# Kernel optimization log

Measured on AMD Instinct MI355X. Metric: run time of the kernel, lower is better.

The kernel has to match this reference:

```python
import jax, jax.numpy as jnp
import numpy as np

T = 2048        # q_len (current chunk)
P = 2048        # past KV cache length
HID = 4096      # hidden_size
H = 32          # num_attention_heads
D = HID // H    # head_dim = 128
THETA = 10000.0


def apply_rope(x, pos):
    # x: [H, T, D], pos: [T] int
    half = D // 2
    inv_freq = 1.0 / (THETA ** (jnp.arange(0, half, dtype=jnp.float32) / half))
    ang = pos.astype(jnp.float32)[:, None] * inv_freq[None, :]      # [T, D/2]
    cos = jnp.concatenate([jnp.cos(ang), jnp.cos(ang)], axis=-1)[None]  # [1, T, D]
    sin = jnp.concatenate([jnp.sin(ang), jnp.sin(ang)], axis=-1)[None]
    rot = jnp.concatenate([-x[..., half:], x[..., :half]], axis=-1)
    return x * cos + rot * sin


def setup_inputs() -> dict:
    key = jax.random.key(0)
    ks = jax.random.split(key, 8)
    s = 1.0 / np.sqrt(HID)
    inp = {
        "hidden_states": jax.random.normal(ks[0], (T, HID), dtype=jnp.float32),
        "attention_mask": jnp.triu(jnp.full((T, T), -jnp.inf, dtype=jnp.float32), k=1),
        "Wq": jax.random.normal(ks[1], (HID, HID), dtype=jnp.float32) * s,
        "Wk": jax.random.normal(ks[2], (HID, HID), dtype=jnp.float32) * s,
        "Wv": jax.random.normal(ks[3], (HID, HID), dtype=jnp.float32) * s,
        "Wo": jax.random.normal(ks[4], (HID, HID), dtype=jnp.float32) * s,
        "past_k": jax.random.normal(ks[5], (H, P, D), dtype=jnp.float32),
        "past_v": jax.random.normal(ks[6], (H, P, D), dtype=jnp.float32),
        "position_ids": P + jnp.arange(T, dtype=jnp.int32),
        "past_length": P,
    }
    return inp


def reference(hidden_states, attention_mask, Wq, Wk, Wv, Wo, past_k, past_v,
              position_ids, past_length):
    # QKV projections -> [H, T, D]
    proj = lambda W: (hidden_states @ W).reshape(T, H, D).transpose(1, 0, 2)
    q, k, v = proj(Wq), proj(Wk), proj(Wv)
    q = apply_rope(q, position_ids)
    k = apply_rope(k, position_ids)

    scale = 1.0 / jnp.sqrt(jnp.float32(D))
    # scores against past cache and current chunk (fp32 softmax, as in source)
    past_dots = (jnp.einsum('htd,hsd->hts', q, past_k) * scale).astype(jnp.float32)
    pmask = jnp.where(jnp.arange(P) < past_length, 0.0, -jnp.inf)  # [P]
    past_dots = past_dots + pmask
    cur = ((jnp.einsum('htd,hsd->hts', q, k) * scale) + attention_mask).astype(jnp.float32)

    # online-softmax merge via logsumexp combination
    past_lse = jax.scipy.special.logsumexp(past_dots, axis=-1, keepdims=True)
    cur_lse = jax.scipy.special.logsumexp(cur, axis=-1, keepdims=True)
    tot_lse = jnp.logaddexp(past_lse, cur_lse)
    pw = jnp.exp(past_dots - tot_lse).astype(q.dtype)
    cw = jnp.exp(cur - tot_lse).astype(q.dtype)

    out = jnp.einsum('hts,hsd->htd', pw, past_v) + jnp.einsum('hts,hsd->htd', cw, v)
    out = jnp.where(past_length == 0,
                    jnp.einsum('hts,hsd->htd', jax.nn.softmax(cur, axis=-1).astype(q.dtype), v),
                    out)
    out = out.transpose(1, 0, 2).reshape(T, HID)   # [T, hidden]
    return out @ Wo
```

## Files before the change

### kernel.cpp

```cpp
#include <hip/hip_runtime.h>
#include <cstdint>
#include <cstddef>

#define T_LEN 2048
#define PAST_MAX 2048
#define HID 4096
#define NHEAD 32
#define DHEAD 128

typedef __bf16 bf16_t;
typedef __bf16 bf16x4 __attribute__((ext_vector_type(4)));
typedef __bf16 bf16x8 __attribute__((ext_vector_type(8)));
typedef float  f32x4  __attribute__((ext_vector_type(4)));
typedef float  f32x16 __attribute__((ext_vector_type(16)));
typedef unsigned int u32x4 __attribute__((ext_vector_type(4)));

__device__ __forceinline__ void gload16(const void* g, void* l){
  __builtin_amdgcn_global_load_lds((const __attribute__((address_space(1))) void*)g,
                                   (__attribute__((address_space(3))) void*)l,
                                   16, 0, 0);
}

__device__ __forceinline__ unsigned pack_bf16(float a, float b){
  const unsigned ua = __builtin_bit_cast(unsigned short, (bf16_t)a);
  const unsigned ub = __builtin_bit_cast(unsigned short, (bf16_t)b);
  return ua | (ub << 16);
}

__global__ void cvt2_k(const float* __restrict__ a, bf16_t* __restrict__ ao,
                       const float* __restrict__ b, bf16_t* __restrict__ bo, int n4){
  int i = blockIdx.x * 256 + threadIdx.x;
  if (i < n4){
    const float4 v = ((const float4*)a)[i];
    bf16x4 o = { (bf16_t)v.x, (bf16_t)v.y, (bf16_t)v.z, (bf16_t)v.w };
    ((bf16x4*)ao)[i] = o;
  } else {
    i -= n4;
    const float4 v = ((const float4*)b)[i];
    bf16x4 o = { (bf16_t)v.x, (bf16_t)v.y, (bf16_t)v.z, (bf16_t)v.w };
    ((bf16x4*)bo)[i] = o;
  }
}

__global__ __launch_bounds__(256) void transpose2_k(const float* __restrict__ in,
                                                    bf16_t* __restrict__ out, int R, int C){
  __shared__ float tile[64][65];
  const int r0 = blockIdx.x << 6, c0 = blockIdx.y << 6;
  const size_t bo = (size_t)blockIdx.z * (size_t)R * (size_t)C;
  const int tx = threadIdx.x & 15, ty = threadIdx.x >> 4;
#pragma unroll
  for (int k = 0; k < 4; ++k){
    const float4 v = *(const float4*)(in + bo + (size_t)(r0 + ty + 16*k) * C + c0 + tx*4);
    float* tp = &tile[ty + 16*k][tx*4];
    tp[0] = v.x; tp[1] = v.y; tp[2] = v.z; tp[3] = v.w;
  }
  __syncthreads();
  const int rr0 = (threadIdx.x & 7) * 8;
  const int ccb = threadIdx.x >> 3;
#pragma unroll
  for (int k = 0; k < 2; ++k){
    const int cc = ccb + 32*k;
    bf16x8 o;
#pragma unroll
    for (int j = 0; j < 8; ++j) o[j] = (bf16_t)tile[rr0 + j][cc];
    *(bf16x8*)(out + bo + (size_t)(c0 + cc) * R + r0 + rr0) = o;
  }
}

__global__ __launch_bounds__(256) void transpose3_k(
    const float* __restrict__ s0, const float* __restrict__ s1, const float* __restrict__ s2,
    bf16_t* __restrict__ d0, bf16_t* __restrict__ d1, bf16_t* __restrict__ d2){
  __shared__ float tile[64][65];
  const float* in = (blockIdx.z == 0) ? s0 : (blockIdx.z == 1) ? s1 : s2;
  bf16_t* out = (blockIdx.z == 0) ? d0 : (blockIdx.z == 1) ? d1 : d2;
  const int r0 = blockIdx.x << 6, c0 = blockIdx.y << 6;
  const int tx = threadIdx.x & 15, ty = threadIdx.x >> 4;
#pragma unroll
  for (int k = 0; k < 4; ++k){
    const float4 v = *(const float4*)(in + (size_t)(r0 + ty + 16*k) * HID + c0 + tx*4);
    float* tp = &tile[ty + 16*k][tx*4];
    tp[0] = v.x; tp[1] = v.y; tp[2] = v.z; tp[3] = v.w;
  }
  __syncthreads();
  const int rr0 = (threadIdx.x & 7) * 8;
  const int ccb = threadIdx.x >> 3;
#pragma unroll
  for (int k = 0; k < 2; ++k){
    const int cc = ccb + 32*k;
    bf16x8 o;
#pragma unroll
    for (int j = 0; j < 8; ++j) o[j] = (bf16_t)tile[rr0 + j][cc];
    *(bf16x8*)(out + (size_t)(c0 + cc) * HID + r0 + rr0) = o;
  }
}

__global__ void ropek_k(bf16_t* __restrict__ K, const int* __restrict__ pos){
  const int idx = blockIdx.x * 256 + threadIdx.x;
  const int i = idx & 63;
  const int t = (idx >> 6) & (T_LEN - 1);
  const int h = idx >> 17;
  const size_t base = ((size_t)h * T_LEN + t) * DHEAD;
  const float p = (float)pos[t];
  const float inv = __expf(-(float)i * 0.14391156605212898f);
  const float ang = p * inv;
  float sn, cs;
  sincosf(ang, &sn, &cs);
  const float b0 = (float)K[base + i], b1 = (float)K[base + i + 64];
  K[base + i]      = (bf16_t)(b0 * cs - b1 * sn);
  K[base + i + 64] = (bf16_t)(b1 * cs + b0 * sn);
}

__global__ __launch_bounds__(512, 1) void gemmqkv256_k(
    const bf16_t* __restrict__ A,
    const bf16_t* __restrict__ B0, const bf16_t* __restrict__ B1, const bf16_t* __restrict__ B2,
    bf16_t* __restrict__ OQ, bf16_t* __restrict__ OK2, bf16_t* __restrict__ OVT, int cpx)
{
  const int bid = blockIdx.x;
  const int wg  = (bid & 7) * cpx + (bid >> 3);
  const int mt  = wg & 7;
  const int nt  = wg >> 3;
  const int z   = nt >> 4;
  const int m0  = mt << 8;
  const int n0  = (nt & 15) << 8;
  const bf16_t* __restrict__ B = (z == 0) ? B0 : (z == 1) ? B1 : B2;

  const int tid = threadIdx.x;
  const int wv = tid >> 6, lane = tid & 63, lm = lane & 15, g = lane >> 4;
  const int wr = wv >> 2, wc = wv & 3;

  __shared__ __align__(16) char smem[131072];

  const f32x4 fzero = {0.f, 0.f, 0.f, 0.f};
  f32x4 acc[8][4];
#pragma unroll
  for (int i = 0; i < 8; ++i)
#pragma unroll
    for (int j = 0; j < 4; ++j) acc[i][j] = fzero;

  int srow[2], schk[2];
#pragma unroll
  for (int i = 0; i < 2; ++i){
    const int c = i * 512 + tid;
    srow[i] = c >> 3;
    schk[i] = (c & 7) ^ (srow[i] & 7);
  }
  const int sdst0 = ((0 * 512 + wv * 64) << 4);
  const int sdst1 = ((1 * 512 + wv * 64) << 4);

  auto stg = [&](int kt, int op){
    if (kt < 64){
      char* dst = smem + (kt & 1) * 65536 + op * 16384;
      const bf16_t* base = (op < 2) ? A + (size_t)(m0 + (op << 7)) * HID
                                    : B + (size_t)(n0 + ((op - 2) << 7)) * HID;
      base += kt * 64;
      gload16(base + (size_t)srow[0] * HID + schk[0] * 8, dst + sdst0);
      gload16(base + (size_t)srow[1] * HID + schk[1] * 8, dst + sdst1);
    }
  };

  const int koff0 = ((g)     ^ (lm & 7)) << 4;
  const int koff1 = ((4 + g) ^ (lm & 7)) << 4;
  const int abase = (wr << 14) + (lm << 7);
  const int bbase = ((2 + (wc >> 1)) << 14) + ((((wc & 1) << 6) + lm) << 7);

  stg(0, 0); stg(0, 1); stg(0, 2); stg(0, 3);
  stg(1, 0); stg(1, 1);
  asm volatile("s_waitcnt vmcnt(4)" ::: "memory");
  __builtin_amdgcn_s_barrier();

  for (int t = 0; t < 64; ++t){
    const char* bufp = smem + (t & 1) * 65536;

    bf16x8 bfr[4][2], afr[4][2];
#pragma unroll
    for (int ni = 0; ni < 4; ++ni){
      bfr[ni][0] = *(const bf16x8*)(bufp + bbase + ni * 2048 + koff0);
      bfr[ni][1] = *(const bf16x8*)(bufp + bbase + ni * 2048 + koff1);
    }
#pragma unroll
    for (int mf = 0; mf < 4; ++mf){
      afr[mf][0] = *(const bf16x8*)(bufp + abase + mf * 2048 + koff0);
      afr[mf][1] = *(const bf16x8*)(bufp + abase + mf * 2048 + koff1);
    }
    stg(t + 1, 2); stg(t + 1, 3);
    __builtin_amdgcn_s_barrier();
    asm volatile("s_waitcnt lgkmcnt(0)" ::: "memory");
    __builtin_amdgcn_s_setprio(1);
#pragma unroll
    for (int kk = 0; kk < 2; ++kk)
#pragma unroll
      for (int mf = 0; mf < 4; ++mf)
#pragma unroll
        for (int ni = 0; ni < 4; ++ni)
          acc[mf][ni] = __builtin_amdgcn_mfma_f32_16x16x32_bf16(afr[mf][kk], bfr[ni][kk], acc[mf][ni], 0, 0, 0);
    __builtin_amdgcn_s_setprio(0);

#pragma unroll
    for (int mf = 0; mf < 4; ++mf){
      afr[mf][0] = *(const bf16x8*)(bufp + abase + (mf + 4) * 2048 + koff0);
      afr[mf][1] = *(const bf16x8*)(bufp + abase + (mf + 4) * 2048 + koff1);
    }
    asm volatile("s_waitcnt lgkmcnt(0)" ::: "memory");
    __builtin_amdgcn_s_barrier();
    stg(t + 2, 0); stg(t + 2, 1);
    if (t + 2 < 64) asm volatile("s_waitcnt vmcnt(4)" ::: "memory");
    else            asm volatile("s_waitcnt vmcnt(0)" ::: "memory");
    __builtin_amdgcn_s_setprio(1);
#pragma unroll
    for (int kk = 0; kk < 2; ++kk)
#pragma unroll
      for (int mf = 0; mf < 4; ++mf)
#pragma unroll
        for (int ni = 0; ni < 4; ++ni)
          acc[mf + 4][ni] = __builtin_amdgcn_mfma_f32_16x16x32_bf16(afr[mf][kk], bfr[ni][kk], acc[mf + 4][ni], 0, 0, 0);
    __builtin_amdgcn_s_setprio(0);
    __builtin_amdgcn_s_barrier();
  }

#pragma unroll
  for (int ni = 0; ni < 4; ++ni){
    const int col = n0 + wc * 64 + ni * 16 + lm;
    const int hh = col >> 7, dd = col & 127;
#pragma unroll
    for (int mf = 0; mf < 8; ++mf)
#pragma unroll
      for (int r = 0; r < 4; ++r){
        const int trow = m0 + wr * 128 + mf * 16 + g * 4 + r;
        const bf16_t v = (bf16_t)acc[mf][ni][r];
        if (z == 2)      OVT[((size_t)hh * DHEAD + dd) * T_LEN + trow] = v;
        else if (z == 1) OK2[((size_t)hh * T_LEN + trow) * DHEAD + dd] = v;
        else             OQ [((size_t)hh * T_LEN + trow) * DHEAD + dd] = v;
      }
  }
}

__global__ __launch_bounds__(512, 1) void gemm4p_k(
    const bf16_t* __restrict__ A, const bf16_t* __restrict__ B,
    float* __restrict__ OF, int cpx)
{
  const int bid = blockIdx.x;
  const int wg  = (bid & 7) * cpx + (bid >> 3);
  const int mt  = wg & 7;
  const int nt  = wg >> 3;
  const int m0  = mt << 8;
  const int n0  = nt << 7;

  const int tid = threadIdx.x;
  const int wv = tid >> 6, lane = tid & 63, lm = lane & 15, g = lane >> 4;
  const int wr = wv >> 1, wc = wv & 1;

  __shared__ __align__(16) char smem[98304];

  const f32x4 fzero = {0.f, 0.f, 0.f, 0.f};
  f32x4 acc[4][4];
#pragma unroll
  for (int i = 0; i < 4; ++i)
#pragma unroll
    for (int j = 0; j < 4; ++j) acc[i][j] = fzero;

  int srow[2], schk[2];
#pragma unroll
  for (int i = 0; i < 2; ++i){
    const int c = i * 512 + tid;
    srow[i] = c >> 3;
    schk[i] = (c & 7) ^ (srow[i] & 7);
  }
  const int sdst0 = ((0 * 512 + wv * 64) << 4);
  const int sdst1 = ((1 * 512 + wv * 64) << 4);

  auto stg = [&](int kt, int op){
    if (kt < 64){
      char* dst = smem + (kt & 1) * 49152 + op * 16384;
      const bf16_t* base = (op < 2) ? A + (size_t)(m0 + (op << 7)) * HID
                                    : B + (size_t)n0 * HID;
      base += kt * 64;
      gload16(base + (size_t)srow[0] * HID + schk[0] * 8, dst + sdst0);
      gload16(base + (size_t)srow[1] * HID + schk[1] * 8, dst + sdst1);
    }
  };

  const int koff0 = ((g)     ^ (lm & 7)) << 4;
  const int koff1 = ((4 + g) ^ (lm & 7)) << 4;
  const int abase = ((wr >> 1) << 14) + ((((wr & 1) << 6) + lm) << 7);
  const int bbase = 32768 + ((((wc << 6)) + lm) << 7);

  bf16x8 bfr[4][2];
  auto dsB = [&](int buf){
    const char* p = smem + buf * 49152 + bbase;
#pragma unroll
    for (int ni = 0; ni < 4; ++ni){
      bfr[ni][0] = *(const bf16x8*)(p + ni * 2048 + koff0);
      bfr[ni][1] = *(const bf16x8*)(p + ni * 2048 + koff1);
    }
  };

  stg(0, 2);
  stg(0, 0); stg(0, 1);
  stg(1, 2);
  asm volatile("s_waitcnt vmcnt(2)" ::: "memory");
  __builtin_amdgcn_s_barrier();

  for (int t = 0; t < 32; ++t){
    const int c0 = 2 * t, c1 = 2 * t + 1;
    const bool last = (t == 31);

#pragma unroll
    for (int half = 0; half < 2; ++half){
      const char* bufp = smem + half * 49152;
      bf16x8 afr[2][2];
      dsB(half);
#pragma unroll
      for (int mf = 0; mf < 2; ++mf){
        afr[mf][0] = *(const bf16x8*)(bufp + abase + mf * 2048 + koff0);
        afr[mf][1] = *(const bf16x8*)(bufp + abase + mf * 2048 + koff1);
      }
      if (half == 0){ stg(c1, 0); stg(c1, 1); }
      else          { stg(c0 + 2, 0); stg(c0 + 2, 1); }
      __builtin_amdgcn_s_barrier();
      asm volatile("s_waitcnt lgkmcnt(0)" ::: "memory");
      __builtin_amdgcn_s_setprio(1);
#pragma unroll
      for (int kk = 0; kk < 2; ++kk)
#pragma unroll
        for (int mf = 0; mf < 2; ++mf)
#pragma unroll
          for (int ni = 0; ni < 4; ++ni)
            acc[mf][ni] = __builtin_amdgcn_mfma_f32_16x16x32_bf16(afr[mf][kk], bfr[ni][kk], acc[mf][ni], 0, 0, 0);
      __builtin_amdgcn_s_setprio(0);
      __builtin_amdgcn_s_barrier();

#pragma unroll
      for (int mf = 0; mf < 2; ++mf){
        afr[mf][0] = *(const bf16x8*)(bufp + abase + (mf + 2) * 2048 + koff0);
        afr[mf][1] = *(const bf16x8*)(bufp + abase + (mf + 2) * 2048 + koff1);
      }
      if (half == 0) stg(c0 + 2, 2);
      else           stg(c1 + 2, 2);
      if (last) asm volatile("s_waitcnt vmcnt(0)" ::: "memory");
      else      asm volatile("s_waitcnt vmcnt(2)" ::: "memory");
      __builtin_amdgcn_s_barrier();
      asm volatile("s_waitcnt lgkmcnt(0)" ::: "memory");
      __builtin_amdgcn_s_setprio(1);
#pragma unroll
      for (int kk = 0; kk < 2; ++kk)
#pragma unroll
        for (int mf = 0; mf < 2; ++mf)
#pragma unroll
          for (int ni = 0; ni < 4; ++ni)
            acc[mf + 2][ni] = __builtin_amdgcn_mfma_f32_16x16x32_bf16(afr[mf][kk], bfr[ni][kk], acc[mf + 2][ni], 0, 0, 0);
      __builtin_amdgcn_s_setprio(0);
      __builtin_amdgcn_s_barrier();
    }
  }

#pragma unroll
  for (int ni = 0; ni < 4; ++ni){
    const int col = n0 + wc * 64 + ni * 16 + lm;
#pragma unroll
    for (int mf = 0; mf < 4; ++mf)
#pragma unroll
      for (int r = 0; r < 4; ++r){
        const int trow = m0 + wr * 64 + mf * 16 + g * 4 + r;
        OF[(size_t)trow * HID + col] = acc[mf][ni][r];
      }
  }
}

__global__ __launch_bounds__(256, 2) void attn2_k(
    const bf16_t* __restrict__ Q,
    const bf16_t* __restrict__ Kc,
    const bf16_t* __restrict__ VTc,
    const bf16_t* __restrict__ Kp,
    const bf16_t* __restrict__ VTp,
    bf16_t* __restrict__ Ctx,
    const int* __restrict__ plen_p,
    const int* __restrict__ pos)
{
  const int bid = blockIdx.x;
  const int xcd = bid & 7;
  const int k   = bid >> 3;
  const int ho  = k >> 4;
  const int qraw= k & 15;
  const int h   = (xcd << 2) | ho;
  const int qb  = (ho & 2) ? (15 - qraw) : qraw;

  const int tid = threadIdx.x;
  const int w = tid >> 6, lane = tid & 63, l31 = lane & 31, hi = lane >> 5;
  const int qw0 = qb * 128 + w * 32;
  const int qrow = qw0 + l31;
  const int plen = plen_p[0];
  const int npast = (plen + 63) >> 6;
  const int NT = npast + 2 * qb + 2;

  __shared__ __align__(16) char smem[65536 + 512];
  float* lred = (float*)(smem + 65536);

  const bf16_t* qbase = Q + ((size_t)h * T_LEN + qrow) * DHEAD;
  bf16x8 qf[8];
#pragma unroll
  for (int dc = 0; dc < 8; ++dc)
    qf[dc] = *(const bf16x8*)(qbase + dc * 16 + 8 * hi);
  {
    const float ppos = (float)pos[qrow];
    const float qs = 0.08838834764831845f;
#pragma unroll
    for (int dc = 0; dc < 4; ++dc)
#pragma unroll
      for (int j = 0; j < 8; ++j){
        const int fi = dc * 16 + 8 * hi + j;
        const float invf = __expf(-(float)fi * 0.14391156605212898f);
        float sn, cs;
        sincosf(ppos * invf, &sn, &cs);
        const float a0 = (float)qf[dc][j], a1 = (float)qf[dc + 4][j];
        qf[dc][j]     = (bf16_t)((a0 * cs - a1 * sn) * qs);
        qf[dc + 4][j] = (bf16_t)((a1 * cs + a0 * sn) * qs);
      }
  }
  __builtin_amdgcn_sched_barrier(0);

  const f32x16 fz = {0.f,0.f,0.f,0.f,0.f,0.f,0.f,0.f,0.f,0.f,0.f,0.f,0.f,0.f,0.f,0.f};
  f32x16 o[4] = {fz, fz, fz, fz};
  float m = -1e30f, l = 0.f;

  auto stage = [&](int t, int buf){
    const bf16_t* kb; const bf16_t* vb;
    if (t < npast){
      const int s0 = t * 64;
      kb = Kp  + ((size_t)h * PAST_MAX + s0) * DHEAD;
      vb = VTp + (size_t)h * DHEAD * PAST_MAX + s0;
    } else {
      const int s0 = (t - npast) * 64;
      kb = Kc  + ((size_t)h * T_LEN + s0) * DHEAD;
      vb = VTc + (size_t)h * DHEAD * T_LEN + s0;
    }
    char* kl = smem + buf * 32768;
    char* vl = kl + 16384;
#pragma unroll
    for (int i = 0; i < 4; ++i){
      const int c = i * 256 + w * 64 + lane;
      const int krow = c >> 4, kcol = c & 15;
      gload16(kb + (size_t)krow * DHEAD + ((kcol ^ (krow & 7)) << 3), kl + (i * 256 + w * 64) * 16);
      const int vrow = c >> 3, vcol = c & 7;
      gload16(vb + (size_t)vrow * 2048 + ((vcol ^ (vrow & 7)) << 3), vl + (i * 256 + w * 64) * 16);
    }
  };

  stage(0, 0);
  __builtin_amdgcn_sched_barrier(0);

  for (int t = 0; t < NT; ++t){
    const int cur = t & 1;
    if (t + 1 < NT){
      stage(t + 1, cur ^ 1);
      asm volatile("s_waitcnt vmcnt(8)" ::: "memory");
    } else {
      asm volatile("s_waitcnt vmcnt(0)" ::: "memory");
    }
    __builtin_amdgcn_sched_barrier(0);
    __builtin_amdgcn_s_barrier();
    __builtin_amdgcn_sched_barrier(0);

    const bool isc = (t >= npast);
    const int s0c = (t - npast) * 64;
    const bool active = !isc || (s0c <= qw0 + 31);

    if (active){
      char* kl = smem + cur * 32768;
      char* vl = kl + 16384;

      f32x16 sacc[2] = {fz, fz};
      __builtin_amdgcn_s_setprio(1);
#pragma unroll
      for (int kvh = 0; kvh < 2; ++kvh){
        const int krow = (kvh << 5) + l31;
        const int kbo = krow << 8;
        const int sw = (krow & 7) << 4;
#pragma unroll
        for (int dc = 0; dc < 8; ++dc){
          const bf16x8 kf = *(const bf16x8*)(kl + kbo + ((dc * 32 + 16 * hi) ^ sw));
          sacc[kvh] = __builtin_amdgcn_mfma_f32_32x32x16_bf16(kf, qf[dc], sacc[kvh], 0, 0, 0);
        }
      }
      __builtin_amdgcn_s_setprio(0);

      const bool mcur  = isc && (s0c + 63 > qw0);
      const bool mpast = !isc && ((t + 1) * 64 > plen);
      float pv[2][16];
      float pm = -1e30f;
      if (mcur | mpast){
#pragma unroll
        for (int kvh = 0; kvh < 2; ++kvh)
#pragma unroll
          for (int r = 0; r < 16; ++r){
            float x = sacc[kvh][r];
            const int kvoff = (kvh << 5) + (r & 3) + 8 * (r >> 2) + 4 * hi;
            if (mcur  && (s0c + kvoff >  qrow)) x = -1e30f;
            if (mpast && (t * 64 + kvoff >= plen)) x = -1e30f;
            pv[kvh][r] = x;
            pm = fmaxf(pm, x);
          }
      } else {
#pragma unroll
        for (int kvh = 0; kvh < 2; ++kvh)
#pragma unroll
          for (int r = 0; r < 16; ++r){
            pv[kvh][r] = sacc[kvh][r];
            pm = fmaxf(pm, sacc[kvh][r]);
          }
      }
      pm = fmaxf(pm, __shfl_xor(pm, 32));

      if (!__all(pm - m <= 8.f)){
        const float mn = fmaxf(m, pm);
        const float corr = __expf(m - mn);
        m = mn;
        l *= corr;
        if (hi == 0) lred[(w << 5) + l31] = corr;
        asm volatile("s_waitcnt lgkmcnt(0)" ::: "memory");
#pragma unroll
        for (int r = 0; r < 16; ++r){
          const float cc = lred[(w << 5) + (r & 3) + 8 * (r >> 2) + 4 * hi];
#pragma unroll
          for (int nb = 0; nb < 4; ++nb) o[nb][r] *= cc;
        }
      }

      float sum = 0.f;
#pragma unroll
      for (int kvh = 0; kvh < 2; ++kvh)
#pragma unroll
        for (int r = 0; r < 16; ++r){
          const float pe = __expf(pv[kvh][r] - m);
          pv[kvh][r] = pe;
          sum += pe;
        }
      sum += __shfl_xor(sum, 32);
      l += sum;

      unsigned wds[2][8];
#pragma unroll
      for (int kvh = 0; kvh < 2; ++kvh)
#pragma unroll
        for (int i = 0; i < 8; ++i)
          wds[kvh][i] = pack_bf16(pv[kvh][2 * i], pv[kvh][2 * i + 1]);

      bf16x8 pf[4];
#pragma unroll
      for (int ks = 0; ks < 4; ++ks){
        const int s = ks & 1, kvh = ks >> 1;
        const unsigned a0 = hi ? wds[kvh][4 * s]     : wds[kvh][4 * s + 2];
        const unsigned a1 = hi ? wds[kvh][4 * s + 1] : wds[kvh][4 * s + 3];
        const unsigned z0 = (unsigned)__shfl_xor((int)a0, 32);
        const unsigned z1 = (unsigned)__shfl_xor((int)a1, 32);
        u32x4 fw;
        fw[0] = hi ? z0 : wds[kvh][4 * s];
        fw[1] = hi ? z1 : wds[kvh][4 * s + 1];
        fw[2] = hi ? wds[kvh][4 * s + 2] : z0;
        fw[3] = hi ? wds[kvh][4 * s + 3] : z1;
        pf[ks] = __builtin_bit_cast(bf16x8, fw);
      }

      __builtin_amdgcn_s_setprio(1);
#pragma unroll
      for (int ks = 0; ks < 4; ++ks)
#pragma unroll
        for (int nb = 0; nb < 4; ++nb){
          const int vrow = (nb << 5) + l31;
          const bf16x8 vf = *(const bf16x8*)(vl + (vrow << 7) + ((ks * 32 + 16 * hi) ^ ((vrow & 7) << 4)));
          o[nb] = __builtin_amdgcn_mfma_f32_32x32x16_bf16(pf[ks], vf, o[nb], 0, 0, 0);
        }
      __builtin_amdgcn_s_setprio(0);
    }
    __builtin_amdgcn_sched_barrier(0);
    __builtin_amdgcn_s_barrier();
  }

  if (hi == 0) lred[(w << 5) + l31] = l;
  asm volatile("s_waitcnt lgkmcnt(0)" ::: "memory");
#pragma unroll
  for (int r = 0; r < 16; ++r){
    const int cr = (r & 3) + 8 * (r >> 2) + 4 * hi;
    const float li = 1.f / lred[(w << 5) + cr];
    const int trow = qw0 + cr;
    bf16_t* cb = Ctx + (size_t)trow * HID + h * DHEAD + l31;
#pragma unroll
    for (int nb = 0; nb < 4; ++nb)
      cb[nb << 5] = (bf16_t)(o[nb][r] * li);
  }
}

extern "C" void kernel_launch(void* const* d_in, const int* in_sizes, int n_in,
                              void* d_out, int out_size, void* d_ws, size_t ws_size,
                              hipStream_t stream)
{
  const float* X   = (const float*)d_in[0];
  const float* Wq  = (const float*)d_in[2];
  const float* Wk  = (const float*)d_in[3];
  const float* Wv  = (const float*)d_in[4];
  const float* Wo  = (const float*)d_in[5];
  const float* PKi = (const float*)d_in[6];
  const float* PVi = (const float*)d_in[7];
  const int* POS   = (const int*)d_in[8];
  const int* PLEN  = (const int*)d_in[9];
  float* OUT = (float*)d_out;

  char* ws = (char*)d_ws;
  const size_t SZ_XB  = (size_t)T_LEN * HID * 2;
  const size_t SZ_W   = (size_t)HID * HID * 2;
  const size_t SZ_HTD = (size_t)NHEAD * T_LEN * DHEAD * 2;

  bf16_t* XB  = (bf16_t*)(ws);
  bf16_t* WT0 = (bf16_t*)(ws + SZ_XB);
  bf16_t* WT1 = (bf16_t*)(ws + SZ_XB + SZ_W);
  bf16_t* WT2 = (bf16_t*)(ws + SZ_XB + 2 * SZ_W);
  char* p = ws + SZ_XB + 3 * SZ_W;
  bf16_t* QB   = (bf16_t*)p; p += SZ_HTD;
  bf16_t* KB   = (bf16_t*)p; p += SZ_HTD;
  bf16_t* VTB  = (bf16_t*)p; p += SZ_HTD;
  bf16_t* KPB  = (bf16_t*)p; p += SZ_HTD;
  bf16_t* VPTB = (bf16_t*)p; p += SZ_HTD;
  bf16_t* CTX  = (bf16_t*)p; p += SZ_HTD;
  bf16_t* WOT  = QB;

  dim3 blk256(256);
  dim3 blk512(512);
  cvt2_k<<<16384, blk256, 0, stream>>>(X, XB, PKi, KPB, T_LEN * HID / 4);
  transpose3_k<<<dim3(64,64,3), blk256, 0, stream>>>(Wq, Wk, Wv, WT0, WT1, WT2);
  transpose2_k<<<dim3(32,2,32), blk256, 0, stream>>>(PVi, VPTB, PAST_MAX, DHEAD);

  gemmqkv256_k<<<384, blk512, 0, stream>>>(XB, WT0, WT1, WT2, QB, KB, VTB, 48);
  ropek_k<<<16384, blk256, 0, stream>>>(KB, POS);
  attn2_k<<<512, blk256, 0, stream>>>(QB, KB, VTB, KPB, VPTB, CTX, PLEN, POS);

  transpose2_k<<<dim3(64,64,1), blk256, 0, stream>>>(Wo, WOT, HID, HID);
  gemm4p_k<<<256, blk512, 0, stream>>>(CTX, WOT, OUT, 32);
}
```

Baseline: 602.0 us.

## Restructure QKV GEMM into 4-stage K32 LDS pipeline with fewer barriers

The fused QKV GEMM kernel moves from a 2-buffer K=64 staging scheme to a 4-buffer ring of K=32 tiles, prefetching three stages ahead. It uses a new swizzled LDS layout and drops one barrier per iteration. The goal is more memory/compute overlap and less barrier stall in the dominant projection GEMM. The cost is twice as many loop iterations, each doing half the MFMA work per sync point, and more intricate vmcnt accounting.

```diff
diff --git a/kernel.cpp b/kernel.cpp
--- a/kernel.cpp
+++ b/kernel.cpp
@@ -110,7 +110,7 @@
   K[base + i + 64] = (bf16_t)(b1 * cs + b0 * sn);
 }
 
-__global__ __launch_bounds__(512, 1) void gemmqkv256_k(
+__global__ __launch_bounds__(512, 1) void gemmqkv8p_k(
     const bf16_t* __restrict__ A,
     const bf16_t* __restrict__ B0, const bf16_t* __restrict__ B1, const bf16_t* __restrict__ B2,
     bf16_t* __restrict__ OQ, bf16_t* __restrict__ OK2, bf16_t* __restrict__ OVT, int cpx)
@@ -137,84 +137,74 @@
 #pragma unroll
     for (int j = 0; j < 4; ++j) acc[i][j] = fzero;
 
-  int srow[2], schk[2];
+  size_t soff[2];
 #pragma unroll
   for (int i = 0; i < 2; ++i){
     const int c = i * 512 + tid;
-    srow[i] = c >> 3;
-    schk[i] = (c & 7) ^ (srow[i] & 7);
-  }
-  const int sdst0 = ((0 * 512 + wv * 64) << 4);
-  const int sdst1 = ((1 * 512 + wv * 64) << 4);
-
-  auto stg = [&](int kt, int op){
-    if (kt < 64){
-      char* dst = smem + (kt & 1) * 65536 + op * 16384;
-      const bf16_t* base = (op < 2) ? A + (size_t)(m0 + (op << 7)) * HID
-                                    : B + (size_t)(n0 + ((op - 2) << 7)) * HID;
-      base += kt * 64;
-      gload16(base + (size_t)srow[0] * HID + schk[0] * 8, dst + sdst0);
-      gload16(base + (size_t)srow[1] * HID + schk[1] * 8, dst + sdst1);
-    }
+    const int d = c >> 3, cc = c & 7;
+    soff[i] = (size_t)(2 * d + (cc >> 2)) * HID + (size_t)((((cc & 3) ^ (d & 3)) << 3));
+  }
+  const bf16_t* Abase = A + (size_t)m0 * HID;
+  const bf16_t* Bbase = B + (size_t)n0 * HID;
+  const int ldst0 = ((0 * 512 + wv * 64) << 4);
+  const int ldst1 = ((1 * 512 + wv * 64) << 4);
+
+  auto stgA = [&](int kt){
+    char* tb = smem + (kt & 3) * 32768;
+    const bf16_t* src = Abase + (size_t)kt * 32;
+    gload16(src + soff[0], tb + ldst0);
+    gload16(src + soff[1], tb + ldst1);
   };
-
-  const int koff0 = ((g)     ^ (lm & 7)) << 4;
-  const int koff1 = ((4 + g) ^ (lm & 7)) << 4;
-  const int abase = (wr << 14) + (lm << 7);
-  const int bbase = ((2 + (wc >> 1)) << 14) + ((((wc & 1) << 6) + lm) << 7);
-
-  stg(0, 0); stg(0, 1); stg(0, 2); stg(0, 3);
-  stg(1, 0); stg(1, 1);
-  asm volatile("s_waitcnt vmcnt(4)" ::: "memory");
+  auto stgB = [&](int kt){
+    char* tb = smem + (kt & 3) * 32768 + 16384;
+    const bf16_t* src = Bbase + (size_t)kt * 32;
+    gload16(src + soff[0], tb + ldst0);
+    gload16(src + soff[1], tb + ldst1);
+  };
+
+  const int fsw = (((g ^ ((lm >> 1) & 3)) << 4)) + ((lm & 1) << 6) + ((lm >> 1) << 7);
+  const int aB_ = (wr << 13) + fsw;
+  const int bB_ = 16384 + (wc << 12) + fsw;
+
+  stgA(0); stgB(0); stgA(1); stgB(1); stgA(2); stgB(2);
+  asm volatile("s_waitcnt vmcnt(8)" ::: "memory");
   __builtin_amdgcn_s_barrier();
 
-  for (int t = 0; t < 64; ++t){
-    const char* bufp = smem + (t & 1) * 65536;
-
-    bf16x8 bfr[4][2], afr[4][2];
-#pragma unroll
-    for (int ni = 0; ni < 4; ++ni){
-      bfr[ni][0] = *(const bf16x8*)(bufp + bbase + ni * 2048 + koff0);
-      bfr[ni][1] = *(const bf16x8*)(bufp + bbase + ni * 2048 + koff1);
-    }
-#pragma unroll
-    for (int mf = 0; mf < 4; ++mf){
-      afr[mf][0] = *(const bf16x8*)(bufp + abase + mf * 2048 + koff0);
-      afr[mf][1] = *(const bf16x8*)(bufp + abase + mf * 2048 + koff1);
-    }
-    stg(t + 1, 2); stg(t + 1, 3);
+  for (int kt = 0; kt < 128; ++kt){
+    const char* tb = smem + (kt & 3) * 32768;
+
+    bf16x8 bfr[4], afr[4];
+#pragma unroll
+    for (int ni = 0; ni < 4; ++ni) bfr[ni] = *(const bf16x8*)(tb + bB_ + ni * 1024);
+#pragma unroll
+    for (int mf = 0; mf < 4; ++mf) afr[mf] = *(const bf16x8*)(tb + aB_ + mf * 1024);
+    if (kt < 125) stgA(kt + 3);
     __builtin_amdgcn_s_barrier();
     asm volatile("s_waitcnt lgkmcnt(0)" ::: "memory");
     __builtin_amdgcn_s_setprio(1);
 #pragma unroll
-    for (int kk = 0; kk < 2; ++kk)
-#pragma unroll
-      for (int mf = 0; mf < 4; ++mf)
-#pragma unroll
-        for (int ni = 0; ni < 4; ++ni)
-          acc[mf][ni] = __builtin_amdgcn_mfma_f32_16x16x32_bf16(afr[mf][kk], bfr[ni][kk], acc[mf][ni], 0, 0, 0);
+    for (int mf = 0; mf < 4; ++mf)
+#pragma unroll
+      for (int ni = 0; ni < 4; ++ni)
+        acc[mf][ni] = __builtin_amdgcn_mfma_f32_16x16x32_bf16(afr[mf], bfr[ni], acc[mf][ni], 0, 0, 0);
     __builtin_amdgcn_s_setprio(0);
 
-#pragma unroll
-    for (int mf = 0; mf < 4; ++mf){
-      afr[mf][0] = *(const bf16x8*)(bufp + abase + (mf + 4) * 2048 + koff0);
-      afr[mf][1] = *(const bf16x8*)(bufp + abase + (mf + 4) * 2048 + koff1);
-    }
+    bf16x8 afr2[4];
+#pragma unroll
+    for (int mf = 0; mf < 4; ++mf) afr2[mf] = *(const bf16x8*)(tb + aB_ + (mf + 4) * 1024);
+    if (kt < 125) stgB(kt + 3);
     asm volatile("s_waitcnt lgkmcnt(0)" ::: "memory");
+    if (kt < 125)       asm volatile("s_waitcnt vmcnt(8)" ::: "memory");
+    else if (kt == 125) asm volatile("s_waitcnt vmcnt(4)" ::: "memory");
+    else                asm volatile("s_waitcnt vmcnt(0)" ::: "memory");
     __builtin_amdgcn_s_barrier();
-    stg(t + 2, 0); stg(t + 2, 1);
-    if (t + 2 < 64) asm volatile("s_waitcnt vmcnt(4)" ::: "memory");
-    else            asm volatile("s_waitcnt vmcnt(0)" ::: "memory");
     __builtin_amdgcn_s_setprio(1);
 #pragma unroll
-    for (int kk = 0; kk < 2; ++kk)
-#pragma unroll
-      for (int mf = 0; mf < 4; ++mf)
-#pragma unroll
-        for (int ni = 0; ni < 4; ++ni)
-          acc[mf + 4][ni] = __builtin_amdgcn_mfma_f32_16x16x32_bf16(afr[mf][kk], bfr[ni][kk], acc[mf + 4][ni], 0, 0, 0);
+    for (int mf = 0; mf < 4; ++mf)
+#pragma unroll
+      for (int ni = 0; ni < 4; ++ni)
+        acc[mf + 4][ni] = __builtin_amdgcn_mfma_f32_16x16x32_bf16(afr2[mf], bfr[ni], acc[mf + 4][ni], 0, 0, 0);
     __builtin_amdgcn_s_setprio(0);
-    __builtin_amdgcn_s_barrier();
   }
 
 #pragma unroll
@@ -628,7 +618,7 @@
   transpose3_k<<<dim3(64,64,3), blk256, 0, stream>>>(Wq, Wk, Wv, WT0, WT1, WT2);
   transpose2_k<<<dim3(32,2,32), blk256, 0, stream>>>(PVi, VPTB, PAST_MAX, DHEAD);
 
-  gemmqkv256_k<<<384, blk512, 0, stream>>>(XB, WT0, WT1, WT2, QB, KB, VTB, 48);
+  gemmqkv8p_k<<<384, blk512, 0, stream>>>(XB, WT0, WT1, WT2, QB, KB, VTB, 48);
   ropek_k<<<16384, blk256, 0, stream>>>(KB, POS);
   attn2_k<<<512, blk256, 0, stream>>>(QB, KB, VTB, KPB, VPTB, CTX, PLEN, POS);
 
```

New measurement: 604.3 us. Within noise of the previous version (+0.4%).
